# Kernel tuning notes

Hardware: AMD Instinct MI355X
Metric: run time of the kernel (lower is better)

## Reference

```python
import jax, jax.numpy as jnp
import numpy as np
from jax import lax


def _conv(x, w, b, stride, pad):
    # x: NCHW, w: OIHW (torch Conv2d layout)
    y = lax.conv_general_dilated(x, w, (stride, stride), ((pad, pad), (pad, pad)),
                                 dimension_numbers=('NCHW', 'OIHW', 'NCHW'))
    return y + b[None, :, None, None]


def _convT(x, w, b):
    # torch ConvTranspose2d(k=4, s=2, p=1); w: (Cin, Cout, 4, 4)
    wf = jnp.flip(w, (2, 3)).transpose(1, 0, 2, 3)  # -> (Cout, Cin, 4, 4)
    y = lax.conv_general_dilated(x, wf, (1, 1), ((2, 2), (2, 2)),
                                 lhs_dilation=(2, 2),
                                 dimension_numbers=('NCHW', 'OIHW', 'NCHW'))
    return y + b[None, :, None, None]


def _res(x, w1, b1, w2, b2):
    # ResBlock: x + conv1x1(relu(conv3x3(relu(x))))
    return x + _conv(jax.nn.relu(_conv(jax.nn.relu(x), w1, b1, 1, 1)), w2, b2, 1, 0)


def setup_inputs() -> dict:
    key = jax.random.key(0)
    ks = iter(jax.random.split(key, 64))

    def p(*shape):
        return jax.random.normal(next(ks), shape, dtype=jnp.float32) * 0.05

    B, C, H, W = 64, 3, 128, 128
    D, K = 32, 512  # embedding_dim, num_embeddings
    inp = {
        'x': jax.random.normal(next(ks), (B, C, H, W), dtype=jnp.float32),
        # encoder
        'ec0_w': p(64, 3, 4, 4), 'ec0_b': p(64),
        'ec1_w': p(128, 64, 4, 4), 'ec1_b': p(128),
        'er1a_w': p(128, 128, 3, 3), 'er1a_b': p(128),
        'er1b_w': p(128, 128, 1, 1), 'er1b_b': p(128),
        'er2a_w': p(128, 128, 3, 3), 'er2a_b': p(128),
        'er2b_w': p(128, 128, 1, 1), 'er2b_b': p(128),
        'ec2_w': p(D, 128, 3, 3), 'ec2_b': p(D),
        # codebook
        'emb': jax.random.normal(next(ks), (K, D), dtype=jnp.float32),
        # decoder
        'dc0_w': p(128, D, 3, 3), 'dc0_b': p(128),
        'dr1a_w': p(128, 128, 3, 3), 'dr1a_b': p(128),
        'dr1b_w': p(128, 128, 1, 1), 'dr1b_b': p(128),
        'dr2a_w': p(128, 128, 3, 3), 'dr2a_b': p(128),
        'dr2b_w': p(128, 128, 1, 1), 'dr2b_b': p(128),
        'dt1_w': p(128, 64, 4, 4), 'dt1_b': p(64),
        'dt2_w': p(64, 3, 4, 4), 'dt2_b': p(3),
    }
    return inp


def reference(x, ec0_w, ec0_b, ec1_w, ec1_b, er1a_w, er1a_b, er1b_w, er1b_b,
              er2a_w, er2a_b, er2b_w, er2b_b, ec2_w, ec2_b, emb,
              dc0_w, dc0_b, dr1a_w, dr1a_b, dr1b_w, dr1b_b,
              dr2a_w, dr2a_b, dr2b_w, dr2b_b, dt1_w, dt1_b, dt2_w, dt2_b):
    # ---- encoder ----
    z = jax.nn.relu(_conv(x, ec0_w, ec0_b, 2, 1))
    z = jax.nn.relu(_conv(z, ec1_w, ec1_b, 2, 1))
    z = _res(z, er1a_w, er1a_b, er1b_w, er1b_b)
    z = _res(z, er2a_w, er2a_b, er2b_w, er2b_b)
    z = _conv(z, ec2_w, ec2_b, 1, 1)  # [B, D, H/4, W/4]
    # ---- vector quantizer ----
    zi = z.transpose(0, 2, 3, 1)                 # NHWC
    flat = zi.reshape(-1, zi.shape[-1])          # [B*H'*W', D]
    d = (jnp.sum(flat * flat, axis=1, keepdims=True)
         + jnp.sum(emb * emb, axis=1)
         - 2.0 * flat @ emb.T)                   # [N, K]
    idx = jnp.argmin(d, axis=1)
    q = jnp.take(emb, idx, axis=0).reshape(zi.shape)  # == one-hot @ emb
    sg = lax.stop_gradient
    vq_loss = jnp.mean((q - sg(zi)) ** 2) + 0.25 * jnp.mean((sg(q) - zi) ** 2)
    q = (zi + sg(q - zi)).transpose(0, 3, 1, 2)  # straight-through, back to NCHW
    # ---- decoder ----
    y = _conv(q, dc0_w, dc0_b, 1, 1)
    y = _res(y, dr1a_w, dr1a_b, dr1b_w, dr1b_b)
    y = _res(y, dr2a_w, dr2a_b, dr2b_w, dr2b_b)
    y = jax.nn.relu(_convT(y, dt1_w, dt1_b))
    y = _convT(y, dt2_w, dt2_b)
    return y, vq_loss
```

## Files before the change

kernel.cpp:

```cpp
#include <hip/hip_runtime.h>


template<int CIN, int COUT, bool RELU_IN, bool RELU_OUT>
__global__ __launch_bounds__(256, 4) void conv3x3_k(
    const float* __restrict__ in, const float* __restrict__ w,
    const float* __restrict__ bias, float* __restrict__ out) {
  __shared__ float wl[CIN * 72];
  const int t = threadIdx.x;
  const int co0 = blockIdx.y * 8;
  for (int i = t; i < CIN * 72; i += 256) {
    const int ci = i / 72, rem = i % 72;
    const int tap = rem >> 3, co = rem & 7;
    wl[i] = w[((co0 + co) * CIN + ci) * 9 + tap];
  }
  __syncthreads();

  const int img = blockIdx.x;
  const int r  = t >> 3;
  const int c4 = t & 7;
  const int w0 = c4 << 2;
  const float* ib = in + (size_t)img * CIN * 1024;

  float acc[4][8];
#pragma unroll
  for (int c = 0; c < 8; ++c) {
    const float b = bias[co0 + c];
#pragma unroll
    for (int p = 0; p < 4; ++p) acc[p][c] = b;
  }

#pragma unroll 1
  for (int ci = 0; ci < CIN; ++ci) {
    const float* ip = ib + (size_t)ci * 1024;
    const float* wp = wl + ci * 72;
    float rin[3][6];
#pragma unroll
    for (int dy = 0; dy < 3; ++dy) {
      const int rr = r - 1 + dy;
      float4 v;
      if ((unsigned)rr < 32u) {
        v = *(const float4*)(ip + (rr << 5) + w0);
        if (RELU_IN) {
          v.x = fmaxf(v.x, 0.f); v.y = fmaxf(v.y, 0.f);
          v.z = fmaxf(v.z, 0.f); v.w = fmaxf(v.w, 0.f);
        }
      } else {
        v.x = 0.f; v.y = 0.f; v.z = 0.f; v.w = 0.f;
      }
      const float lft = __shfl_up(v.w, 1);
      const float rgt = __shfl_down(v.x, 1);
      rin[dy][0] = (c4 > 0) ? lft : 0.f;
      rin[dy][1] = v.x; rin[dy][2] = v.y; rin[dy][3] = v.z; rin[dy][4] = v.w;
      rin[dy][5] = (c4 < 7) ? rgt : 0.f;
    }
#pragma unroll
    for (int dy = 0; dy < 3; ++dy)
#pragma unroll
      for (int dx = 0; dx < 3; ++dx) {
        float wv[8];
        *(float4*)(wv)     = *(const float4*)(wp + (dy * 3 + dx) * 8);
        *(float4*)(wv + 4) = *(const float4*)(wp + (dy * 3 + dx) * 8 + 4);
#pragma unroll
        for (int p = 0; p < 4; ++p) {
          const float xv = rin[dy][dx + p];
#pragma unroll
          for (int c = 0; c < 8; ++c) acc[p][c] = fmaf(xv, wv[c], acc[p][c]);
        }
      }
  }
#pragma unroll
  for (int c = 0; c < 8; ++c) {
    float4 o;
    o.x = acc[0][c]; o.y = acc[1][c]; o.z = acc[2][c]; o.w = acc[3][c];
    if (RELU_OUT) {
      o.x = fmaxf(o.x, 0.f); o.y = fmaxf(o.y, 0.f);
      o.z = fmaxf(o.z, 0.f); o.w = fmaxf(o.w, 0.f);
    }
    *(float4*)(out + (((size_t)img * COUT + co0 + c) * 32 + r) * 32 + w0) = o;
  }
}

template<int CIN, int COUT, int HOUT, bool RELU_OUT>
__global__ __launch_bounds__(256) void conv4x4s2_k(
    const float* __restrict__ in, const float* __restrict__ w,
    const float* __restrict__ bias, float* __restrict__ out) {
  constexpr int HIN = HOUT * 2;
  constexpr int PW = HOUT / 32;
  constexpr int PPI = PW * PW;
  __shared__ float wl[CIN * 128];
  const int t = threadIdx.x;
  const int co0 = blockIdx.y * 8;
  for (int i = t; i < CIN * 128; i += 256) {
    const int ci = i >> 7, rem = i & 127;
    const int tap = rem >> 3, co = rem & 7;
    wl[i] = w[((co0 + co) * CIN + ci) * 16 + tap];
  }
  __syncthreads();
  const int piece = blockIdx.x * 2 + (t >> 7);
  const int img = piece / PPI;
  const int prc = piece % PPI;
  const int pr = prc / PW, pc = prc % PW;
  const int tid = t & 127;
  const int r  = (tid >> 2) + pr * 32;
  const int w0 = ((tid & 3) << 3) + pc * 32;
  float acc[8][8];
#pragma unroll
  for (int c = 0; c < 8; ++c) {
    const float b = bias[co0 + c];
#pragma unroll
    for (int p = 0; p < 8; ++p) acc[p][c] = b;
  }
  const float* ib = in + (size_t)img * CIN * HIN * HIN;
#pragma unroll 1
  for (int ci = 0; ci < CIN; ++ci) {
    const float* ip = ib + (size_t)ci * HIN * HIN;
    const float* wp = wl + ci * 128;
#pragma unroll
    for (int ky = 0; ky < 4; ++ky) {
      const int rr = 2 * r - 1 + ky;
      const bool rok = (unsigned)rr < (unsigned)HIN;
      const float* rp = ip + rr * HIN;
      float rowv[18];
      if (rok) {
        rowv[0] = (2 * w0 - 1 >= 0) ? rp[2 * w0 - 1] : 0.f;
#pragma unroll
        for (int q = 0; q < 4; ++q)
          *(float4*)(&rowv[1 + 4 * q]) = *(const float4*)(rp + 2 * w0 + 4 * q);
        rowv[17] = (2 * w0 + 16 < HIN) ? rp[2 * w0 + 16] : 0.f;
      } else {
#pragma unroll
        for (int cc = 0; cc < 18; ++cc) rowv[cc] = 0.f;
      }
#pragma unroll
      for (int kx = 0; kx < 4; ++kx) {
        float wv[8];
        *(float4*)(wv)     = *(const float4*)(wp + (ky * 4 + kx) * 8);
        *(float4*)(wv + 4) = *(const float4*)(wp + (ky * 4 + kx) * 8 + 4);
#pragma unroll
        for (int p = 0; p < 8; ++p) {
          const float xv = rowv[2 * p + kx];
#pragma unroll
          for (int c = 0; c < 8; ++c) acc[p][c] = fmaf(xv, wv[c], acc[p][c]);
        }
      }
    }
  }
#pragma unroll
  for (int c = 0; c < 8; ++c) {
    float* op = out + (((size_t)img * COUT + co0 + c) * HOUT + r) * HOUT + w0;
#pragma unroll
    for (int p = 0; p < 8; ++p) {
      float v = acc[p][c];
      if (RELU_OUT) v = fmaxf(v, 0.f);
      op[p] = v;
    }
  }
}

template<int CIN, int COUT, int COCH, int HOUT, bool RELU_OUT>
__global__ __launch_bounds__(256) void convT4x4s2_k(
    const float* __restrict__ in, const float* __restrict__ w,
    const float* __restrict__ bias, float* __restrict__ out) {
  constexpr int HIN = HOUT / 2;
  constexpr int GPR = HOUT / 16;
  constexpr int TPP = 32 * GPR;
  constexpr int PPB = 256 / TPP;
  constexpr int PPI = HOUT / 32;
  __shared__ float wl[CIN * 16 * COCH];
  const int t = threadIdx.x;
  const int co0 = blockIdx.y * COCH;
  for (int i = t; i < CIN * 16 * COCH; i += 256) {
    const int ci = i / (16 * COCH);
    const int rem = i % (16 * COCH);
    const int tap = rem / COCH, co = rem % COCH;
    float v = 0.f;
    if (co0 + co < COUT) v = w[((size_t)ci * COUT + co0 + co) * 16 + tap];
    wl[i] = v;
  }
  __syncthreads();
  const int piece = blockIdx.x * PPB + t / TPP;
  const int img = piece / PPI;
  const int pr = piece % PPI;
  const int tid = t % TPP;
  const int r  = tid / GPR + pr * 32;
  const int w0 = (tid % GPR) * 16;
  float acc[16][COCH];
#pragma unroll
  for (int c = 0; c < COCH; ++c) {
    const float b = (co0 + c < COUT) ? bias[co0 + c] : 0.f;
#pragma unroll
    for (int m = 0; m < 16; ++m) acc[m][c] = b;
  }
  const float* ib = in + (size_t)img * CIN * HIN * HIN;
  const int kyb = (r + 1) & 1;
  const int hi0 = (r + 1 - kyb) >> 1;
#pragma unroll 1
  for (int ci = 0; ci < CIN; ++ci) {
    const float* ip = ib + (size_t)ci * HIN * HIN;
    float rin[2][10];
#pragma unroll
    for (int jy = 0; jy < 2; ++jy) {
      const int hh = hi0 - jy;
      const bool rok = (unsigned)hh < (unsigned)HIN;
      const float* rp = ip + hh * HIN;
      const int c0 = (w0 >> 1);
      if (rok) {
        rin[jy][0] = (c0 > 0) ? rp[c0 - 1] : 0.f;
        *(float4*)(&rin[jy][1]) = *(const float4*)(rp + c0);
        *(float4*)(&rin[jy][5]) = *(const float4*)(rp + c0 + 4);
        rin[jy][9] = (c0 + 8 < HIN) ? rp[c0 + 8] : 0.f;
      } else {
#pragma unroll
        for (int cc = 0; cc < 10; ++cc) rin[jy][cc] = 0.f;
      }
    }
    const float* wp = wl + ci * 16 * COCH;
#pragma unroll
    for (int jy = 0; jy < 2; ++jy) {
      const int ky = kyb + 2 * jy;
#pragma unroll
      for (int kx = 0; kx < 4; ++kx) {
        const int p = (kx + 1) & 1;
        const int idx0 = ((p + 1 - kx) >> 1) + 1;
        float wv[COCH];
#pragma unroll
        for (int c = 0; c < COCH; c += 4)
          *(float4*)(wv + c) = *(const float4*)(wp + (ky * 4 + kx) * COCH + c);
#pragma unroll
        for (int m = 0; m < 8; ++m) {
          const float xv = rin[jy][idx0 + m];
#pragma unroll
          for (int c = 0; c < COCH; ++c)
            acc[2 * m + p][c] = fmaf(xv, wv[c], acc[2 * m + p][c]);
        }
      }
    }
  }
#pragma unroll
  for (int c = 0; c < COCH; ++c) {
    if (co0 + c < COUT) {
      float* op = out + (((size_t)img * COUT + co0 + c) * HOUT + r) * HOUT + w0;
#pragma unroll
      for (int m = 0; m < 16; ++m) {
        float v = acc[m][c];
        if (RELU_OUT) v = fmaxf(v, 0.f);
        op[m] = v;
      }
    }
  }
}

__global__ __launch_bounds__(256) void conv1x1res_k(
    const float* __restrict__ in, const float* __restrict__ w,
    const float* __restrict__ bias, float* __restrict__ io) {
  __shared__ float wl[128 * 16];
  const int t = threadIdx.x;
  const int co0 = blockIdx.y * 16;
  for (int i = t; i < 2048; i += 256) {
    const int ci = i >> 4, co = i & 15;
    wl[i] = w[(co0 + co) * 128 + ci];
  }
  __syncthreads();
  const int img = blockIdx.x;
  float acc[4][16];
#pragma unroll
  for (int c = 0; c < 16; ++c) {
    const float b = bias[co0 + c];
#pragma unroll
    for (int p = 0; p < 4; ++p) acc[p][c] = b;
  }
  const float4* ip = (const float4*)(in + (size_t)img * 131072);
#pragma unroll 4
  for (int ci = 0; ci < 128; ++ci) {
    float xv[4];
    *(float4*)xv = ip[ci * 256 + t];
    float wv[16];
#pragma unroll
    for (int c = 0; c < 16; c += 4)
      *(float4*)(wv + c) = *(const float4*)(wl + ci * 16 + c);
#pragma unroll
    for (int p = 0; p < 4; ++p)
#pragma unroll
      for (int c = 0; c < 16; ++c) acc[p][c] = fmaf(xv[p], wv[c], acc[p][c]);
  }
  float4* iop = (float4*)(io + (size_t)img * 131072);
#pragma unroll
  for (int c = 0; c < 16; ++c) {
    float4 v = iop[(co0 + c) * 256 + t];
    v.x += acc[0][c]; v.y += acc[1][c]; v.z += acc[2][c]; v.w += acc[3][c];
    iop[(co0 + c) * 256 + t] = v;
  }
}

__global__ __launch_bounds__(256) void vq_prep_k(const float* __restrict__ emb,
    float* __restrict__ e2, float* __restrict__ lossAcc) {
  const int k = blockIdx.x * 256 + threadIdx.x;
  if (k < 512) {
    float s = 0.f;
#pragma unroll
    for (int d = 0; d < 32; ++d) { const float v = emb[k * 32 + d]; s = fmaf(v, v, s); }
    e2[k] = s;
  }
  if (k == 0) lossAcc[0] = 0.f;
}

__global__ __launch_bounds__(256) void vq_k(
    const float* __restrict__ z, const float* __restrict__ emb,
    const float* __restrict__ e2, float* __restrict__ q,
    float* __restrict__ lossAcc) {
  const int n = blockIdx.x * 256 + threadIdx.x;
  const int img = n >> 10, pos = n & 1023;
  const float* zp = z + (size_t)img * 32768 + pos;
  float zv[32];
#pragma unroll
  for (int d = 0; d < 32; ++d) zv[d] = zp[d * 1024];
  float best = 3.4e38f;
  int bk = 0;
  const float4* ev = (const float4*)emb;
#pragma unroll 2
  for (int k = 0; k < 512; ++k) {
    float d0 = 0.f, d1 = 0.f, d2 = 0.f, d3 = 0.f;
#pragma unroll
    for (int j = 0; j < 8; ++j) {
      const float4 e = ev[k * 8 + j];
      d0 = fmaf(zv[4 * j + 0], e.x, d0);
      d1 = fmaf(zv[4 * j + 1], e.y, d1);
      d2 = fmaf(zv[4 * j + 2], e.z, d2);
      d3 = fmaf(zv[4 * j + 3], e.w, d3);
    }
    const float dist = fmaf(-2.f, (d0 + d1) + (d2 + d3), e2[k]);
    if (dist < best) { best = dist; bk = k; }
  }
  float ls = 0.f;
  float* qp = q + (size_t)img * 32768 + pos;
#pragma unroll
  for (int d = 0; d < 32; ++d) {
    const float qd = emb[bk * 32 + d];
    qp[d * 1024] = qd;
    const float df = qd - zv[d];
    ls = fmaf(df, df, ls);
  }
#pragma unroll
  for (int off = 32; off > 0; off >>= 1) ls += __shfl_down(ls, off);
  __shared__ float wred[4];
  const int lane = threadIdx.x & 63, wid = threadIdx.x >> 6;
  if (lane == 0) wred[wid] = ls;
  __syncthreads();
  if (threadIdx.x == 0) atomicAdd(lossAcc, (wred[0] + wred[1]) + (wred[2] + wred[3]));
}

__global__ void loss_fin_k(const float* __restrict__ lossAcc, float* __restrict__ o) {
  o[0] = 1.25f * lossAcc[0] * (1.0f / 2097152.0f);
}

extern "C" void kernel_launch(void* const* d_in, const int* in_sizes, int n_in,
                              void* d_out, int out_size, void* d_ws, size_t ws_size,
                              hipStream_t stream) {
  (void)in_sizes; (void)n_in; (void)out_size; (void)ws_size;
  const float* x      = (const float*)d_in[0];
  const float* ec0_w  = (const float*)d_in[1];  const float* ec0_b = (const float*)d_in[2];
  const float* ec1_w  = (const float*)d_in[3];  const float* ec1_b = (const float*)d_in[4];
  const float* er1a_w = (const float*)d_in[5];  const float* er1a_b = (const float*)d_in[6];
  const float* er1b_w = (const float*)d_in[7];  const float* er1b_b = (const float*)d_in[8];
  const float* er2a_w = (const float*)d_in[9];  const float* er2a_b = (const float*)d_in[10];
  const float* er2b_w = (const float*)d_in[11]; const float* er2b_b = (const float*)d_in[12];
  const float* ec2_w  = (const float*)d_in[13]; const float* ec2_b = (const float*)d_in[14];
  const float* emb    = (const float*)d_in[15];
  const float* dc0_w  = (const float*)d_in[16]; const float* dc0_b = (const float*)d_in[17];
  const float* dr1a_w = (const float*)d_in[18]; const float* dr1a_b = (const float*)d_in[19];
  const float* dr1b_w = (const float*)d_in[20]; const float* dr1b_b = (const float*)d_in[21];
  const float* dr2a_w = (const float*)d_in[22]; const float* dr2a_b = (const float*)d_in[23];
  const float* dr2b_w = (const float*)d_in[24]; const float* dr2b_b = (const float*)d_in[25];
  const float* dt1_w  = (const float*)d_in[26]; const float* dt1_b = (const float*)d_in[27];
  const float* dt2_w  = (const float*)d_in[28]; const float* dt2_b = (const float*)d_in[29];
  float* out = (float*)d_out;
  float* ws  = (float*)d_ws;

  float* A    = ws;
  float* B    = ws + 16777216;
  float* C    = A;
  float* Z    = A + 8388608;
  float* Q    = A + 10485760;
  float* E2   = ws + 25165824;
  float* LACC = ws + 25166336;

  conv4x4s2_k<3, 64, 64, true><<<dim3(128, 8), 256, 0, stream>>>(x, ec0_w, ec0_b, A);
  conv4x4s2_k<64, 128, 32, true><<<dim3(32, 16), 256, 0, stream>>>(A, ec1_w, ec1_b, B);
  conv3x3_k<128, 128, true, true><<<dim3(64, 16), 256, 0, stream>>>(B, er1a_w, er1a_b, C);
  conv1x1res_k<<<dim3(64, 8), 256, 0, stream>>>(C, er1b_w, er1b_b, B);
  conv3x3_k<128, 128, true, true><<<dim3(64, 16), 256, 0, stream>>>(B, er2a_w, er2a_b, C);
  conv1x1res_k<<<dim3(64, 8), 256, 0, stream>>>(C, er2b_w, er2b_b, B);
  conv3x3_k<128, 32, false, false><<<dim3(64, 4), 256, 0, stream>>>(B, ec2_w, ec2_b, Z);
  vq_prep_k<<<2, 256, 0, stream>>>(emb, E2, LACC);
  vq_k<<<256, 256, 0, stream>>>(Z, emb, E2, Q, LACC);
  conv3x3_k<32, 128, false, false><<<dim3(64, 16), 256, 0, stream>>>(Q, dc0_w, dc0_b, B);
  conv3x3_k<128, 128, true, true><<<dim3(64, 16), 256, 0, stream>>>(B, dr1a_w, dr1a_b, C);
  conv1x1res_k<<<dim3(64, 8), 256, 0, stream>>>(C, dr1b_w, dr1b_b, B);
  conv3x3_k<128, 128, true, true><<<dim3(64, 16), 256, 0, stream>>>(B, dr2a_w, dr2a_b, C);
  conv1x1res_k<<<dim3(64, 8), 256, 0, stream>>>(C, dr2b_w, dr2b_b, B);
  convT4x4s2_k<128, 64, 8, 64, true><<<dim3(64, 8), 256, 0, stream>>>(B, dt1_w, dt1_b, A);
  convT4x4s2_k<64, 3, 4, 128, false><<<dim3(256, 1), 256, 0, stream>>>(A, dt2_w, dt2_b, out);
  loss_fin_k<<<1, 1, 0, stream>>>(LACC, out + 3145728);
}
```

Measured before the change: 2.200 ms.

## Prefetch next-channel rows in conv3x3 and chunk convT weights for occupancy

In the 3x3 conv kernel, the input rows for the next channel are now loaded into registers while the current channel's FMAs run, which hides global-memory latency. The transposed-conv kernel now stages weights in shared memory in input-channel chunks, halving the LDS footprint when it exceeds 8192 floats. It also adds a minimum-occupancy launch bound of four blocks. The tradeoff is higher register pressure from the prefetch buffers and the bound, which may cause spills, plus an extra barrier per chunk in the transposed conv.

```diff
diff --git a/kernel.cpp b/kernel.cpp
--- a/kernel.cpp
+++ b/kernel.cpp
@@ -29,11 +29,8 @@
     for (int p = 0; p < 4; ++p) acc[p][c] = b;
   }
 
-#pragma unroll 1
-  for (int ci = 0; ci < CIN; ++ci) {
+  auto loadrows = [&](int ci, float4* dst) {
     const float* ip = ib + (size_t)ci * 1024;
-    const float* wp = wl + ci * 72;
-    float rin[3][6];
 #pragma unroll
     for (int dy = 0; dy < 3; ++dy) {
       const int rr = r - 1 + dy;
@@ -47,6 +44,20 @@
       } else {
         v.x = 0.f; v.y = 0.f; v.z = 0.f; v.w = 0.f;
       }
+      dst[dy] = v;
+    }
+  };
+
+  float4 cur[3], nxt[3];
+  loadrows(0, cur);
+#pragma unroll 1
+  for (int ci = 0; ci < CIN; ++ci) {
+    if (ci + 1 < CIN) loadrows(ci + 1, nxt);
+    const float* wp = wl + ci * 72;
+    float rin[3][6];
+#pragma unroll
+    for (int dy = 0; dy < 3; ++dy) {
+      const float4 v = cur[dy];
       const float lft = __shfl_up(v.w, 1);
       const float rgt = __shfl_down(v.x, 1);
       rin[dy][0] = (c4 > 0) ? lft : 0.f;
@@ -67,6 +78,8 @@
           for (int c = 0; c < 8; ++c) acc[p][c] = fmaf(xv, wv[c], acc[p][c]);
         }
       }
+#pragma unroll
+    for (int dy = 0; dy < 3; ++dy) cur[dy] = nxt[dy];
   }
 #pragma unroll
   for (int c = 0; c < 8; ++c) {
@@ -158,7 +171,7 @@
 }
 
 template<int CIN, int COUT, int COCH, int HOUT, bool RELU_OUT>
-__global__ __launch_bounds__(256) void convT4x4s2_k(
+__global__ __launch_bounds__(256, 4) void convT4x4s2_k(
     const float* __restrict__ in, const float* __restrict__ w,
     const float* __restrict__ bias, float* __restrict__ out) {
   constexpr int HIN = HOUT / 2;
@@ -166,18 +179,10 @@
   constexpr int TPP = 32 * GPR;
   constexpr int PPB = 256 / TPP;
   constexpr int PPI = HOUT / 32;
-  __shared__ float wl[CIN * 16 * COCH];
+  constexpr int CI_CHUNK = (CIN * 16 * COCH <= 8192) ? CIN : (CIN / 2);
+  __shared__ float wl[CI_CHUNK * 16 * COCH];
   const int t = threadIdx.x;
   const int co0 = blockIdx.y * COCH;
-  for (int i = t; i < CIN * 16 * COCH; i += 256) {
-    const int ci = i / (16 * COCH);
-    const int rem = i % (16 * COCH);
-    const int tap = rem / COCH, co = rem % COCH;
-    float v = 0.f;
-    if (co0 + co < COUT) v = w[((size_t)ci * COUT + co0 + co) * 16 + tap];
-    wl[i] = v;
-  }
-  __syncthreads();
   const int piece = blockIdx.x * PPB + t / TPP;
   const int img = piece / PPI;
   const int pr = piece % PPI;
@@ -195,43 +200,57 @@
   const int kyb = (r + 1) & 1;
   const int hi0 = (r + 1 - kyb) >> 1;
 #pragma unroll 1
-  for (int ci = 0; ci < CIN; ++ci) {
-    const float* ip = ib + (size_t)ci * HIN * HIN;
-    float rin[2][10];
-#pragma unroll
-    for (int jy = 0; jy < 2; ++jy) {
-      const int hh = hi0 - jy;
-      const bool rok = (unsigned)hh < (unsigned)HIN;
-      const float* rp = ip + hh * HIN;
-      const int c0 = (w0 >> 1);
-      if (rok) {
-        rin[jy][0] = (c0 > 0) ? rp[c0 - 1] : 0.f;
-        *(float4*)(&rin[jy][1]) = *(const float4*)(rp + c0);
-        *(float4*)(&rin[jy][5]) = *(const float4*)(rp + c0 + 4);
-        rin[jy][9] = (c0 + 8 < HIN) ? rp[c0 + 8] : 0.f;
-      } else {
-#pragma unroll
-        for (int cc = 0; cc < 10; ++cc) rin[jy][cc] = 0.f;
-      }
-    }
-    const float* wp = wl + ci * 16 * COCH;
-#pragma unroll
-    for (int jy = 0; jy < 2; ++jy) {
-      const int ky = kyb + 2 * jy;
-#pragma unroll
-      for (int kx = 0; kx < 4; ++kx) {
-        const int p = (kx + 1) & 1;
-        const int idx0 = ((p + 1 - kx) >> 1) + 1;
-        float wv[COCH];
-#pragma unroll
-        for (int c = 0; c < COCH; c += 4)
-          *(float4*)(wv + c) = *(const float4*)(wp + (ky * 4 + kx) * COCH + c);
-#pragma unroll
-        for (int m = 0; m < 8; ++m) {
-          const float xv = rin[jy][idx0 + m];
-#pragma unroll
-          for (int c = 0; c < COCH; ++c)
-            acc[2 * m + p][c] = fmaf(xv, wv[c], acc[2 * m + p][c]);
+  for (int ci0 = 0; ci0 < CIN; ci0 += CI_CHUNK) {
+    if (ci0 > 0) __syncthreads();
+    for (int i = t; i < CI_CHUNK * 16 * COCH; i += 256) {
+      const int cil = i / (16 * COCH);
+      const int rem = i % (16 * COCH);
+      const int tap = rem / COCH, co = rem % COCH;
+      float v = 0.f;
+      if (co0 + co < COUT) v = w[((size_t)(ci0 + cil) * COUT + co0 + co) * 16 + tap];
+      wl[i] = v;
+    }
+    __syncthreads();
+#pragma unroll 1
+    for (int cil = 0; cil < CI_CHUNK; ++cil) {
+      const int ci = ci0 + cil;
+      const float* ip = ib + (size_t)ci * HIN * HIN;
+      float rin[2][10];
+#pragma unroll
+      for (int jy = 0; jy < 2; ++jy) {
+        const int hh = hi0 - jy;
+        const bool rok = (unsigned)hh < (unsigned)HIN;
+        const float* rp = ip + hh * HIN;
+        const int c0 = (w0 >> 1);
+        if (rok) {
+          rin[jy][0] = (c0 > 0) ? rp[c0 - 1] : 0.f;
+          *(float4*)(&rin[jy][1]) = *(const float4*)(rp + c0);
+          *(float4*)(&rin[jy][5]) = *(const float4*)(rp + c0 + 4);
+          rin[jy][9] = (c0 + 8 < HIN) ? rp[c0 + 8] : 0.f;
+        } else {
+#pragma unroll
+          for (int cc = 0; cc < 10; ++cc) rin[jy][cc] = 0.f;
+        }
+      }
+      const float* wp = wl + cil * 16 * COCH;
+#pragma unroll
+      for (int jy = 0; jy < 2; ++jy) {
+        const int ky = kyb + 2 * jy;
+#pragma unroll
+        for (int kx = 0; kx < 4; ++kx) {
+          const int p = (kx + 1) & 1;
+          const int idx0 = ((p + 1 - kx) >> 1) + 1;
+          float wv[COCH];
+#pragma unroll
+          for (int c = 0; c < COCH; c += 4)
+            *(float4*)(wv + c) = *(const float4*)(wp + (ky * 4 + kx) * COCH + c);
+#pragma unroll
+          for (int m = 0; m < 8; ++m) {
+            const float xv = rin[jy][idx0 + m];
+#pragma unroll
+            for (int c = 0; c < COCH; ++c)
+              acc[2 * m + p][c] = fmaf(xv, wv[c], acc[2 * m + p][c]);
+          }
         }
       }
     }
```

After: 5.798 ms. 2.64x slower.
